# Kernel tuning notes

Hardware: AMD Instinct MI355X
Metric: run time of the kernel (lower is better)

Reference implementation:

```python
import jax, jax.numpy as jnp
import numpy as np
from jax import lax

EPS = 2.220446049250313e-16  # np.finfo(float).eps, used in SparseDispatcher.combine
TOP_K = 2
LOSS_COEF = 1e-2


def _conv7(x, w, groups):
    # x: [B,C,H,W], w: [O, C//groups, 7, 7], 'same' padding
    return lax.conv_general_dilated(
        x, w, window_strides=(1, 1), padding=[(3, 3), (3, 3)],
        dimension_numbers=("NCHW", "OIHW", "NCHW"), feature_group_count=groups)


def setup_inputs() -> dict:
    key = jax.random.key(0)
    ks = jax.random.split(key, 8)
    B, C, H, E = 16, 64, 128, 8
    x = jax.random.normal(ks[0], (B, C, H, H), dtype=jnp.float32)
    # router: Conv2d(dim, 1, 7, padding=3)
    router_w = jax.random.normal(ks[1], (1, C, 7, 7), dtype=jnp.float32) * 0.05
    router_b = jnp.zeros((1,), dtype=jnp.float32)
    # gating weight: [weight_h*weight_h, num_experts] (small random so top-k is meaningful)
    w_gate = jax.random.normal(ks[2], (H * H, E), dtype=jnp.float32) * 0.01
    # experts: depthwise Conv2d(dim, dim, 7, groups=dim) per expert
    expert_w = jax.random.normal(ks[3], (E, C, 1, 7, 7), dtype=jnp.float32) * 0.05
    expert_b = jnp.zeros((E, C), dtype=jnp.float32)
    # shared expert: same depthwise conv
    shared_w = jax.random.normal(ks[4], (C, 1, 7, 7), dtype=jnp.float32) * 0.05
    shared_b = jnp.zeros((C,), dtype=jnp.float32)
    return dict(x=x, router_w=router_w, router_b=router_b, w_gate=w_gate,
                expert_w=expert_w, expert_b=expert_b,
                shared_w=shared_w, shared_b=shared_b)


def reference(x, router_w, router_b, w_gate, expert_w, expert_b, shared_w, shared_b):
    B, C, H, W = x.shape
    E = w_gate.shape[1]

    # ---- router + top-k gating (noisy_gating=False path) ----
    r = _conv7(x, router_w, groups=1) + router_b[None, :, None, None]   # [B,1,H,W]
    r_flat = r.reshape(B, H * W)                                        # [B,HW]
    logits = r_flat @ w_gate                                            # [B,E]
    top_logits, top_idx = lax.top_k(logits, min(TOP_K + 1, E))
    top_k_gates = jax.nn.softmax(top_logits[:, :TOP_K], axis=1)         # [B,k]
    gates = jnp.zeros((B, E), logits.dtype).at[
        jnp.arange(B)[:, None], top_idx[:, :TOP_K]].set(top_k_gates)     # [B,E]

    importance = gates.sum(0)
    load = (gates > 0).sum(0).astype(jnp.float32)

    def cv_sq(v):  # torch .var() is unbiased -> ddof=1
        return jnp.var(v, ddof=1) / (jnp.mean(v) ** 2 + 1e-10)

    loss = (cv_sq(importance) + cv_sq(load)) * LOSS_COEF

    # ---- experts: depthwise 7x7 conv per expert ----
    out = jax.vmap(lambda w, b: _conv7(x, w, C) + b[None, :, None, None])(
        expert_w, expert_b)                                             # [E,B,C,H,W]
    out = out.reshape(E, B, C, H * W).transpose(0, 1, 3, 2)             # [E,B,HW,C]

    # ---- SparseDispatcher.combine (multiply_by_gates=False): log-sum-exp over
    # selected experts only. Dense masked form == gather/scatter form exactly. ----
    mask = (gates > 0).T[:, :, None, None].astype(out.dtype)            # [E,B,1,1]
    combined = jnp.sum(jnp.exp(out) * mask, axis=0)                     # [B,HW,C]
    combined = jnp.where(combined == 0, EPS, combined)
    y = jnp.log(combined)

    # ---- shared expert ----
    shared = (_conv7(x, shared_w, C) + shared_b[None, :, None, None])
    shared = shared.reshape(B, C, H * W).transpose(0, 2, 1)             # [B,HW,C]

    return y + shared, loss
```

## Files before the change

### kernel.cpp

```cpp
#include <hip/hip_runtime.h>
#include <hip/hip_bf16.h>

#define B_  16
#define C_  64
#define H_  128
#define W_  128
#define HW_ (H_*W_)
#define E_  8

#define WS_LOGITS 0
#define WS_SEL    128

__global__ void k_sentinel(float* out, float v){
    if (blockIdx.x == 0 && threadIdx.x == 0) out[0] = v;
}

#define R_TH 16
#define R_TW 64
#define R_HH (R_TH+6)
#define R_HW (R_TW+6)
#define R_LS 76
#define R_HN (R_HH*R_HW)
#define RG_CH 8
#define RG_N  8

__device__ __forceinline__ void r_stage(const float* __restrict__ xc, float* dst,
                                        int row0, int col0, int tid){
    for (int i = tid; i < R_HN; i += 256){
        int hr = i / R_HW, hc = i - hr*R_HW;
        int gr = row0 + hr - 3, gc = col0 + hc - 3;
        float v = 0.f;
        if ((unsigned)gr < (unsigned)H_ && (unsigned)gc < (unsigned)W_)
            v = xc[gr*W_+gc];
        dst[hr*R_LS+hc] = v;
    }
}

__global__ __launch_bounds__(256) void k1p(const float* __restrict__ x,
                                           const float* __restrict__ rw,
                                           const float* __restrict__ rb,
                                           float* __restrict__ part){
    __shared__ __align__(16) float tile[2][R_HH*R_LS];

    int id = blockIdx.x;
    int g   = id & 7; id >>= 3;
    int txt = id & 1; id >>= 1;
    int tyt = id & 7; id >>= 3;
    int b   = id;
    int row0 = tyt*R_TH, col0 = txt*R_TW;
    int tx = threadIdx.x & 15, ty = threadIdx.x >> 4;
    int row  = row0 + ty;
    int colb = col0 + 4*tx;

    const float* xg  = x  + ((size_t)(b*C_) + g*RG_CH)*HW_;
    const float* wgr = rw + g*RG_CH*49;

    float acc[4] = {0.f,0.f,0.f,0.f};

    r_stage(xg, tile[0], row0, col0, threadIdx.x);
    __syncthreads();

    for (int ch = 0; ch < RG_CH; ++ch){
        if (ch + 1 < RG_CH)
            r_stage(xg + (size_t)(ch+1)*HW_, tile[(ch+1)&1], row0, col0, threadIdx.x);

        const float* wr = wgr + ch*49;
        const float* tb = tile[ch&1];
        #pragma unroll
        for (int ky = 0; ky < 7; ++ky){
            const float* trp = &tb[(ty+ky)*R_LS + 4*tx];
            float4 va = *(const float4*)(trp);
            float4 vb = *(const float4*)(trp+4);
            float2 vc = *(const float2*)(trp+8);
            float win[10] = {va.x,va.y,va.z,va.w, vb.x,vb.y,vb.z,vb.w, vc.x,vc.y};
            #pragma unroll
            for (int kx = 0; kx < 7; ++kx){
                float w = wr[ky*7+kx];
                acc[0] += w*win[kx+0];
                acc[1] += w*win[kx+1];
                acc[2] += w*win[kx+2];
                acc[3] += w*win[kx+3];
            }
        }
        __syncthreads();
    }

    if (g == 0){
        float rbv = rb[0];
        acc[0]+=rbv; acc[1]+=rbv; acc[2]+=rbv; acc[3]+=rbv;
    }
    float* pr = part + (size_t)g*(B_*HW_);
    size_t base = (size_t)b*HW_ + (size_t)row*W_ + colb;
    #pragma unroll
    for (int p = 0; p < 4; ++p) pr[base+p] = acc[p];
}

__global__ __launch_bounds__(256) void kg(const float* __restrict__ part,
                                          const float* __restrict__ wg,
                                          float* __restrict__ logits){
    __shared__ float red[256];
    int b = blockIdx.x >> 3, e = blockIdx.x & 7;
    const float* p0 = part + (size_t)b*HW_;
    float s = 0.f;
    for (int hw = threadIdx.x; hw < HW_; hw += 256){
        float rv = 0.f;
        #pragma unroll
        for (int gg = 0; gg < RG_N; ++gg)
            rv += p0[hw + (size_t)gg*(B_*HW_)];
        s += rv * wg[(size_t)hw*E_ + e];
    }
    red[threadIdx.x] = s;
    __syncthreads();
    for (int off = 128; off > 0; off >>= 1){
        if (threadIdx.x < off) red[threadIdx.x] += red[threadIdx.x + off];
        __syncthreads();
    }
    if (threadIdx.x == 0) logits[b*E_+e] = red[0];
}

__global__ void k2_gating(const float* __restrict__ logits,
                          int* __restrict__ sel,
                          float* __restrict__ out){
    __shared__ float g1s[B_], g2s[B_];
    __shared__ int   i1s[B_], i2s[B_];
    __shared__ float impS[E_], cntS[E_];
    int t = threadIdx.x;
    if (t < B_){
        const float* l = logits + t*E_;
        int i1 = 0;
        #pragma unroll
        for (int e = 1; e < E_; ++e) if (l[e] > l[i1]) i1 = e;
        int i2 = (i1 == 0) ? 1 : 0;
        #pragma unroll
        for (int e = 0; e < E_; ++e) if (e != i1 && l[e] > l[i2]) i2 = e;
        float ex = expf(l[i2] - l[i1]);
        float g1 = 1.f/(1.f+ex), g2 = ex/(1.f+ex);
        sel[t] = i1; sel[B_ + t] = i2;
        g1s[t] = g1; g2s[t] = g2; i1s[t] = i1; i2s[t] = i2;
    }
    __syncthreads();
    if (t < E_){
        float im = 0.f, cn = 0.f;
        #pragma unroll
        for (int bb = 0; bb < B_; ++bb){
            im += (i1s[bb]==t ? g1s[bb] : 0.f) + (i2s[bb]==t ? g2s[bb] : 0.f);
            cn += (i1s[bb]==t ? 1.f : 0.f)     + (i2s[bb]==t ? 1.f : 0.f);
        }
        impS[t] = im; cntS[t] = cn;
    }
    __syncthreads();
    if (t == 0){
        float m1 = 0.f, m2 = 0.f;
        for (int e = 0; e < E_; ++e){ m1 += impS[e]; m2 += cntS[e]; }
        m1 *= (1.f/E_); m2 *= (1.f/E_);
        float v1 = 0.f, v2 = 0.f;
        for (int e = 0; e < E_; ++e){
            float d1 = impS[e] - m1; v1 += d1*d1;
            float d2 = cntS[e] - m2; v2 += d2*d2;
        }
        v1 *= (1.f/(E_-1)); v2 *= (1.f/(E_-1));
        float loss = (v1/(m1*m1 + 1e-10f) + v2/(m2*m2 + 1e-10f)) * 0.01f;
        out[(size_t)B_*HW_*C_] = loss;
    }
}

#define C3_NCH 8
#define C3_CS  28
#define C3_CHS (22*C3_CS)
#define C3_WST 56
#define C3_TN  (C3_NCH*22*22)
#define C3_WN  (3*C3_NCH*C3_WST)

__global__ __launch_bounds__(256) void k3_tiled(const float* __restrict__ x,
                                                const float* __restrict__ ew,
                                                const float* __restrict__ eb,
                                                const float* __restrict__ sw,
                                                const float* __restrict__ sb,
                                                const int* __restrict__ sel,
                                                float* __restrict__ out){
    __shared__ __align__(16) float tile[C3_NCH*C3_CHS];
    __shared__ __align__(16) float wbuf[C3_WN];

    int id = blockIdx.x;
    int cx = id & 7; id >>= 3;
    int cy = id & 7; id >>= 3;
    int b  = id;
    int r0 = cy*16, c0 = cx*16;

    int c8   = threadIdx.x & 7;
    int slot = threadIdx.x >> 3;
    int trow = slot >> 1;
    int colt = (slot & 1) * 8;

    int e1 = sel[b], e2 = sel[B_ + b];

    for (int k = 0; k < 8; ++k){
        int cc0 = k*C3_NCH;
        __syncthreads();
        for (int i = threadIdx.x; i < C3_TN; i += 256){
            int ci = i / 484; int rem = i - ci*484;
            int hr = rem / 22, hc = rem - hr*22;
            int gr = r0 + hr - 3, gc = c0 + hc - 3;
            float v = 0.f;
            if ((unsigned)gr < (unsigned)H_ && (unsigned)gc < (unsigned)W_)
                v = x[((size_t)(b*C_ + cc0 + ci))*HW_ + gr*W_ + gc];
            tile[ci*C3_CHS + hr*C3_CS + hc] = v;
        }
        for (int i = threadIdx.x; i < C3_WN; i += 256){
            int which = i / 448;
            int rem = i - which*448;
            int wc = rem / C3_WST;
            int tt = rem - wc*C3_WST;
            int ky = tt >> 3, kx = tt & 7;
            float v = 0.f;
            if (kx < 7){
                int tap = ky*7 + kx;
                if (which == 0)      v = ew[((size_t)(e1*C_ + cc0 + wc))*49 + tap];
                else if (which == 1) v = ew[((size_t)(e2*C_ + cc0 + wc))*49 + tap];
                else                 v = sw[((size_t)(cc0 + wc))*49 + tap];
            }
            wbuf[i] = v;
        }
        __syncthreads();

        float a1[8], a2[8], a3[8];
        #pragma unroll
        for (int c = 0; c < 8; ++c){ a1[c]=0.f; a2[c]=0.f; a3[c]=0.f; }

        const float* tb = tile + c8*C3_CHS;
        #pragma unroll
        for (int ky = 0; ky < 7; ++ky){
            const float* trp = tb + (trow+ky)*C3_CS + colt;
            float win[16];
            #pragma unroll
            for (int q = 0; q < 4; ++q){
                float4 v4 = *(const float4*)(trp + 4*q);
                win[4*q+0]=v4.x; win[4*q+1]=v4.y; win[4*q+2]=v4.z; win[4*q+3]=v4.w;
            }
            float u1[7], u2[7], u3[7];
            { const float* wp = wbuf + (0*C3_NCH + c8)*C3_WST + ky*8;
              float4 a = *(const float4*)wp, c4 = *(const float4*)(wp+4);
              u1[0]=a.x;u1[1]=a.y;u1[2]=a.z;u1[3]=a.w;u1[4]=c4.x;u1[5]=c4.y;u1[6]=c4.z; }
            { const float* wp = wbuf + (1*C3_NCH + c8)*C3_WST + ky*8;
              float4 a = *(const float4*)wp, c4 = *(const float4*)(wp+4);
              u2[0]=a.x;u2[1]=a.y;u2[2]=a.z;u2[3]=a.w;u2[4]=c4.x;u2[5]=c4.y;u2[6]=c4.z; }
            { const float* wp = wbuf + (2*C3_NCH + c8)*C3_WST + ky*8;
              float4 a = *(const float4*)wp, c4 = *(const float4*)(wp+4);
              u3[0]=a.x;u3[1]=a.y;u3[2]=a.z;u3[3]=a.w;u3[4]=c4.x;u3[5]=c4.y;u3[6]=c4.z; }

            #pragma unroll
            for (int c = 0; c < 8; ++c){
                #pragma unroll
                for (int kx = 0; kx < 7; ++kx){
                    float xv = win[c+kx];
                    a1[c] += u1[kx]*xv;
                    a2[c] += u2[kx]*xv;
                    a3[c] += u3[kx]*xv;
                }
            }
        }

        float b1 = eb[e1*C_ + cc0 + c8];
        float b2 = eb[e2*C_ + cc0 + c8];
        float b3 = sb[cc0 + c8];
        size_t obase = ((size_t)b*HW_ + (size_t)(r0+trow)*W_ + (c0+colt))*C_ + cc0 + c8;
        #pragma unroll
        for (int c = 0; c < 8; ++c){
            float o1 = a1[c] + b1;
            float o2 = a2[c] + b2;
            float o3 = a3[c] + b3;
            float v = __expf(o1) + __expf(o2);
            if (v == 0.f) v = 2.220446049250313e-16f;
            out[obase + (size_t)c*C_] = __logf(v) + o3;
        }
    }
}

extern "C" void kernel_launch(void* const* d_in, const int* in_sizes, int n_in,
                              void* d_out, int out_size, void* d_ws, size_t ws_size,
                              hipStream_t stream) {
    float* out = (float*)d_out;

    static const int exp_sizes[8] = {16777216, 3136, 1, 131072, 25088, 512, 3136, 64};
    if (n_in != 8){ k_sentinel<<<1,64,0,stream>>>(out, 500.f); return; }
    for (int i = 0; i < 8; ++i){
        if (in_sizes[i] != exp_sizes[i]){
            k_sentinel<<<1,64,0,stream>>>(out, 600.f + 8.f*i); return;
        }
    }
    if (out_size != 16777217){ k_sentinel<<<1,64,0,stream>>>(out, 800.f); return; }
    if (ws_size < (size_t)(WS_SEL + 64)*4){ k_sentinel<<<1,64,0,stream>>>(out, 900.f); return; }

    const float* x  = (const float*)d_in[0];
    const float* rw = (const float*)d_in[1];
    const float* rb = (const float*)d_in[2];
    const float* wg = (const float*)d_in[3];
    const float* ew = (const float*)d_in[4];
    const float* eb = (const float*)d_in[5];
    const float* sw = (const float*)d_in[6];
    const float* sb = (const float*)d_in[7];
    float* wsf = (float*)d_ws;

    k1p<<<2048, 256, 0, stream>>>(x, rw, rb, out);
    kg<<<128, 256, 0, stream>>>(out, wg, wsf + WS_LOGITS);
    k2_gating<<<1, 64, 0, stream>>>(wsf + WS_LOGITS, (int*)(wsf + WS_SEL), out);
    k3_tiled<<<1024, 256, 0, stream>>>(x, ew, eb, sw, sb,
                                       (const int*)(wsf + WS_SEL), out);
}
```

Measured before the change: 347.1 us.

## Fuse gating matvec into router conv and split expert conv over channel halves

The router conv kernel now multiplies its outputs by the gating weights in place and reduces them to per-block partial logits, removing the separate kg kernel and the round trip of the full router map through global memory. The gating kernel sums the 128 partials per batch before top-k. The expert conv kernel splits its channel loop across two blocks to double the grid, and its shared-memory strides are padded, likely to reduce bank conflicts. The cost is redundant halo and weight staging for each half and a serial partial sum in a single block.

Measured after the change: 311.6 us. -10.2%, faster.

```diff
diff --git a/kernel.cpp b/kernel.cpp
--- a/kernel.cpp
+++ b/kernel.cpp
@@ -10,6 +10,7 @@
 
 #define WS_LOGITS 0
 #define WS_SEL    128
+#define WS_PART   256
 
 __global__ void k_sentinel(float* out, float v){
     if (blockIdx.x == 0 && threadIdx.x == 0) out[0] = v;
@@ -39,8 +40,10 @@
 __global__ __launch_bounds__(256) void k1p(const float* __restrict__ x,
                                            const float* __restrict__ rw,
                                            const float* __restrict__ rb,
-                                           float* __restrict__ part){
+                                           const float* __restrict__ wg,
+                                           float* __restrict__ partial){
     __shared__ __align__(16) float tile[2][R_HH*R_LS];
+    __shared__ float pred[4][E_];
 
     int id = blockIdx.x;
     int g   = id & 7; id >>= 3;
@@ -89,44 +92,56 @@
         float rbv = rb[0];
         acc[0]+=rbv; acc[1]+=rbv; acc[2]+=rbv; acc[3]+=rbv;
     }
-    float* pr = part + (size_t)g*(B_*HW_);
-    size_t base = (size_t)b*HW_ + (size_t)row*W_ + colb;
+
+    const float* wrow = wg + (size_t)(row*W_ + colb)*E_;
+    float pl[E_];
     #pragma unroll
-    for (int p = 0; p < 4; ++p) pr[base+p] = acc[p];
-}
-
-__global__ __launch_bounds__(256) void kg(const float* __restrict__ part,
-                                          const float* __restrict__ wg,
-                                          float* __restrict__ logits){
-    __shared__ float red[256];
-    int b = blockIdx.x >> 3, e = blockIdx.x & 7;
-    const float* p0 = part + (size_t)b*HW_;
-    float s = 0.f;
-    for (int hw = threadIdx.x; hw < HW_; hw += 256){
-        float rv = 0.f;
-        #pragma unroll
-        for (int gg = 0; gg < RG_N; ++gg)
-            rv += p0[hw + (size_t)gg*(B_*HW_)];
-        s += rv * wg[(size_t)hw*E_ + e];
-    }
-    red[threadIdx.x] = s;
-    __syncthreads();
-    for (int off = 128; off > 0; off >>= 1){
-        if (threadIdx.x < off) red[threadIdx.x] += red[threadIdx.x + off];
-        __syncthreads();
-    }
-    if (threadIdx.x == 0) logits[b*E_+e] = red[0];
-}
-
-__global__ void k2_gating(const float* __restrict__ logits,
+    for (int e = 0; e < E_; ++e) pl[e] = 0.f;
+    #pragma unroll
+    for (int p = 0; p < 4; ++p){
+        float4 wa = *(const float4*)(wrow + p*E_);
+        float4 wb = *(const float4*)(wrow + p*E_ + 4);
+        float a = acc[p];
+        pl[0] += a*wa.x; pl[1] += a*wa.y; pl[2] += a*wa.z; pl[3] += a*wa.w;
+        pl[4] += a*wb.x; pl[5] += a*wb.y; pl[6] += a*wb.z; pl[7] += a*wb.w;
+    }
+    #pragma unroll
+    for (int off = 32; off > 0; off >>= 1){
+        #pragma unroll
+        for (int e = 0; e < E_; ++e) pl[e] += __shfl_down(pl[e], off, 64);
+    }
+    int lane = threadIdx.x & 63, wv = threadIdx.x >> 6;
+    if (lane == 0){
+        #pragma unroll
+        for (int e = 0; e < E_; ++e) pred[wv][e] = pl[e];
+    }
+    __syncthreads();
+    if (threadIdx.x < E_){
+        int e = threadIdx.x;
+        float s = pred[0][e] + pred[1][e] + pred[2][e] + pred[3][e];
+        partial[(size_t)blockIdx.x*E_ + e] = s;
+    }
+}
+
+__global__ void k2_gating(const float* __restrict__ partial,
                           int* __restrict__ sel,
                           float* __restrict__ out){
+    __shared__ float lg[B_*E_];
     __shared__ float g1s[B_], g2s[B_];
     __shared__ int   i1s[B_], i2s[B_];
     __shared__ float impS[E_], cntS[E_];
     int t = threadIdx.x;
+    if (t < B_*E_){
+        int b = t >> 3, e = t & 7;
+        const float* pp = partial + ((size_t)b*128)*E_ + e;
+        float s = 0.f;
+        #pragma unroll 4
+        for (int j = 0; j < 128; ++j) s += pp[(size_t)j*E_];
+        lg[t] = s;
+    }
+    __syncthreads();
     if (t < B_){
-        const float* l = logits + t*E_;
+        const float* l = lg + t*E_;
         int i1 = 0;
         #pragma unroll
         for (int e = 1; e < E_; ++e) if (l[e] > l[i1]) i1 = e;
@@ -166,8 +181,8 @@
 
 #define C3_NCH 8
 #define C3_CS  28
-#define C3_CHS (22*C3_CS)
-#define C3_WST 56
+#define C3_CHS 620
+#define C3_WST 60
 #define C3_TN  (C3_NCH*22*22)
 #define C3_WN  (3*C3_NCH*C3_WST)
 
@@ -182,6 +197,7 @@
     __shared__ __align__(16) float wbuf[C3_WN];
 
     int id = blockIdx.x;
+    int half = id & 1; id >>= 1;
     int cx = id & 7; id >>= 3;
     int cy = id & 7; id >>= 3;
     int b  = id;
@@ -194,8 +210,8 @@
 
     int e1 = sel[b], e2 = sel[B_ + b];
 
-    for (int k = 0; k < 8; ++k){
-        int cc0 = k*C3_NCH;
+    for (int kk = 0; kk < 4; ++kk){
+        int cc0 = (half*4 + kk)*C3_NCH;
         __syncthreads();
         for (int i = threadIdx.x; i < C3_TN; i += 256){
             int ci = i / 484; int rem = i - ci*484;
@@ -207,13 +223,13 @@
             tile[ci*C3_CHS + hr*C3_CS + hc] = v;
         }
         for (int i = threadIdx.x; i < C3_WN; i += 256){
-            int which = i / 448;
-            int rem = i - which*448;
+            int which = i / (C3_NCH*C3_WST);
+            int rem = i - which*(C3_NCH*C3_WST);
             int wc = rem / C3_WST;
             int tt = rem - wc*C3_WST;
             int ky = tt >> 3, kx = tt & 7;
             float v = 0.f;
-            if (kx < 7){
+            if (ky < 7 && kx < 7){
                 int tap = ky*7 + kx;
                 if (which == 0)      v = ew[((size_t)(e1*C_ + cc0 + wc))*49 + tap];
                 else if (which == 1) v = ew[((size_t)(e2*C_ + cc0 + wc))*49 + tap];
@@ -289,7 +305,7 @@
         }
     }
     if (out_size != 16777217){ k_sentinel<<<1,64,0,stream>>>(out, 800.f); return; }
-    if (ws_size < (size_t)(WS_SEL + 64)*4){ k_sentinel<<<1,64,0,stream>>>(out, 900.f); return; }
+    if (ws_size < (size_t)(WS_PART + 2048*E_)*4){ k_sentinel<<<1,64,0,stream>>>(out, 900.f); return; }
 
     const float* x  = (const float*)d_in[0];
     const float* rw = (const float*)d_in[1];
@@ -301,9 +317,8 @@
     const float* sb = (const float*)d_in[7];
     float* wsf = (float*)d_ws;
 
-    k1p<<<2048, 256, 0, stream>>>(x, rw, rb, out);
-    kg<<<128, 256, 0, stream>>>(out, wg, wsf + WS_LOGITS);
-    k2_gating<<<1, 64, 0, stream>>>(wsf + WS_LOGITS, (int*)(wsf + WS_SEL), out);
-    k3_tiled<<<1024, 256, 0, stream>>>(x, ew, eb, sw, sb,
+    k1p<<<2048, 256, 0, stream>>>(x, rw, rb, wg, wsf + WS_PART);
+    k2_gating<<<1, 256, 0, stream>>>(wsf + WS_PART, (int*)(wsf + WS_SEL), out);
+    k3_tiled<<<2048, 256, 0, stream>>>(x, ew, eb, sw, sb,
                                        (const int*)(wsf + WS_SEL), out);
 }
```
